# Kernel tuning notes

Measured on AMD Instinct MI355X. Metric: run time of the kernel, lower is better.

The kernel has to match this reference:

```python
import jax, jax.numpy as jnp
import numpy as np

SENTINEL = 1 << 20  # fill value for padded unique rows; far outside real coord range


def setup_inputs() -> dict:
    key = jax.random.key(0)
    k1, k2, k3, k4, k5, kw = jax.random.split(key, 6)
    M, C = 400000, 128
    voxel_features = jax.random.normal(k1, (M, C), dtype=jnp.float32)
    # coords: (batch_idx, z, y, x)
    b = jax.random.randint(k2, (M, 1), 0, 4, dtype=jnp.int32)
    z = jax.random.randint(k3, (M, 1), 0, 40, dtype=jnp.int32)
    y = jax.random.randint(k4, (M, 1), 0, 1024, dtype=jnp.int32)
    x = jax.random.randint(k5, (M, 1), 0, 1024, dtype=jnp.int32)
    voxel_coords = jnp.concatenate([b, z, y, x], axis=1)
    # layer-1 (stride=1) uses a random (in,out) matmul weight in the original;
    # materialize it as a fixed parameter for determinism.
    W0 = jax.random.normal(kw, (C, C), dtype=jnp.float32)
    return {"voxel_features": voxel_features, "voxel_coords": voxel_coords,
            "W0": W0, "batch_size": 4}


def _forward(voxel_features, W0, voxel_coords):
    M = voxel_features.shape[0]
    # layer 1: stride=1 -> relu then matmul (placeholder dense path)
    feats = jnp.maximum(voxel_features, 0.0) @ W0  # (M, 128)
    coords = voxel_coords
    # layers 2 and 3: stride=2 -> quantize coords (ALL 4 cols, incl. batch idx,
    # matching the original), unique, scatter-add features, relu
    for _ in range(2):
        coords = jnp.floor(coords.astype(jnp.float32) / 2.0).astype(jnp.int32)
        uniq, inv = jnp.unique(coords, axis=0, return_inverse=True,
                               size=M, fill_value=SENTINEL)
        inv = inv.reshape(-1)
        feats = jax.ops.segment_sum(feats, inv, num_segments=M)  # fused scatter-add
        feats = jnp.maximum(feats, 0.0)
        coords = uniq
    # rows beyond the true unique count are zero padding (sentinel coords)
    return feats


def reference(voxel_features, voxel_coords, W0, batch_size):
    return _forward(voxel_features, W0, voxel_coords)
```

## Files before the change

kernel.cpp:

```cpp
#include <hip/hip_runtime.h>
#include <stdint.h>

#define C 128

typedef __attribute__((ext_vector_type(8))) short bf16x8;
typedef __attribute__((ext_vector_type(4))) float f32x4;
typedef __attribute__((ext_vector_type(2))) float f32x2;

__device__ __forceinline__ uint32_t f2bf1(float f) {
    uint32_t u = __float_as_uint(f);
    return (u + 0x7FFFu + ((u >> 16) & 1u)) >> 16;
}


__global__ __launch_bounds__(512) void zeroconv_kernel(
    uint4* __restrict__ zbase, int nquads,
    const float* __restrict__ W, ushort* __restrict__ Wt, int nzb) {
    int b = blockIdx.x, t = threadIdx.x;
    if (b < nzb) {
        int i = b * 512 + t;
        if (i < nquads) zbase[i] = (uint4){0u, 0u, 0u, 0u};
    } else {
        int id = (b - nzb) * 512 + t;
        int n = id >> 7, k = id & 127;
        Wt[id] = (ushort)f2bf1(W[k * C + n]);
    }
}

__global__ __launch_bounds__(512) void mark_kernel(
    const int* __restrict__ coords, uint32_t* __restrict__ bm1,
    uint32_t* __restrict__ bm2, int M) {
    int i = blockIdx.x * 512 + threadIdx.x;
    if (i >= M) return;
    int bb = coords[4*i+0], z = coords[4*i+1], y = coords[4*i+2], x = coords[4*i+3];
    uint32_t k1 = ((uint32_t)(bb>>1)<<23) | ((uint32_t)(z>>1)<<18) |
                  ((uint32_t)(y>>1)<<9)  | (uint32_t)(x>>1);
    uint32_t k2 = ((uint32_t)(z>>2)<<16) | ((uint32_t)(y>>2)<<8) | (uint32_t)(x>>2);
    atomicOr(&bm1[k1>>5], 1u << (k1 & 31));
    atomicOr(&bm2[k2>>5], 1u << (k2 & 31));
}

__device__ __forceinline__ void bscan1_512(const uint32_t* bm, uint32_t* bs,
                                           int blk, uint32_t* s, int t) {
    int base = blk * 1024 + t * 2;
    uint32_t sum = __popc(bm[base]) + __popc(bm[base+1]);
    s[t] = sum;
    __syncthreads();
    for (int off = 256; off > 0; off >>= 1) {
        if (t < off) s[t] += s[t + off];
        __syncthreads();
    }
    if (t == 0) bs[blk] = s[0];
}

__device__ __forceinline__ void bscan3_512(const uint32_t* bm, const uint32_t* bs,
                                           uint32_t* wp, int blk, uint32_t* s, int t) {
    int base = blk * 1024 + t * 2;
    uint32_t p0 = __popc(bm[base]), p1 = __popc(bm[base+1]);
    uint32_t sum = p0 + p1;
    s[t] = sum;
    __syncthreads();
    for (int off = 1; off < 512; off <<= 1) {
        uint32_t add = (t >= off) ? s[t - off] : 0u;
        __syncthreads();
        s[t] += add;
        __syncthreads();
    }
    uint32_t ex = s[t] - sum + bs[blk];
    wp[base]   = ex;
    wp[base+1] = ex + p0;
}

__device__ __forceinline__ void blksum_scan_512(uint32_t* bs, uint32_t* total,
                                                int nb, uint32_t* s, int t) {
    uint32_t v = (t < nb) ? bs[t] : 0u;
    s[t] = v;
    __syncthreads();
    for (int off = 1; off < 512; off <<= 1) {
        uint32_t add = (t >= off) ? s[t - off] : 0u;
        __syncthreads();
        s[t] += add;
        __syncthreads();
    }
    if (t < nb) bs[t] = s[t] - v;
    if (t == nb - 1) *total = s[t];
}

__device__ __forceinline__ void vscan1_512(const uint32_t* v, uint32_t* bs,
                                           int blk, int n, uint32_t* s, int t) {
    int base = blk * 1024 + t * 2;
    uint32_t sum = 0;
    if (base     < n) sum += v[base];
    if (base + 1 < n) sum += v[base+1];
    s[t] = sum;
    __syncthreads();
    for (int off = 256; off > 0; off >>= 1) {
        if (t < off) s[t] += s[t + off];
        __syncthreads();
    }
    if (t == 0) bs[blk] = s[0];
}

__device__ __forceinline__ void vscan3_512(const uint32_t* v, const uint32_t* bs,
                                           uint32_t* ex_out, int blk, int n,
                                           uint32_t* s, int t) {
    int base = blk * 1024 + t * 2;
    uint32_t p0 = (base     < n) ? v[base]   : 0u;
    uint32_t p1 = (base + 1 < n) ? v[base+1] : 0u;
    uint32_t sum = p0 + p1;
    s[t] = sum;
    __syncthreads();
    for (int off = 1; off < 512; off <<= 1) {
        uint32_t add = (t >= off) ? s[t - off] : 0u;
        __syncthreads();
        s[t] += add;
        __syncthreads();
    }
    uint32_t e = s[t] - sum + bs[blk];
    if (base     < n) ex_out[base]   = e;
    if (base + 1 < n) ex_out[base+1] = e + p0;
}

__global__ __launch_bounds__(512) void mscan1_kernel(
    const uint32_t* __restrict__ bm1, uint32_t* __restrict__ bs1,
    const uint32_t* __restrict__ bm2, uint32_t* __restrict__ bs2) {
    __shared__ uint32_t s[512];
    int b = blockIdx.x, t = threadIdx.x;
    if (b < 512) bscan1_512(bm1, bs1, b, s, t);
    else         bscan1_512(bm2, bs2, b - 512, s, t);
}

__global__ __launch_bounds__(512) void mscan2_kernel(
    uint32_t* __restrict__ bs1, uint32_t* __restrict__ bs2,
    uint32_t* __restrict__ totals) {
    __shared__ uint32_t s[512];
    int t = threadIdx.x;
    if (blockIdx.x == 0) blksum_scan_512(bs1, &totals[0], 512, s, t);
    else                 blksum_scan_512(bs2, &totals[1], 32,  s, t);
}

__global__ __launch_bounds__(512) void mscan3_kernel(
    const uint32_t* __restrict__ bm1, const uint32_t* __restrict__ bs1,
    uint32_t* __restrict__ wp1,
    const uint32_t* __restrict__ bm2, const uint32_t* __restrict__ bs2,
    uint32_t* __restrict__ wp2) {
    __shared__ uint32_t s[512];
    int b = blockIdx.x, t = threadIdx.x;
    if (b < 512) bscan3_512(bm1, bs1, wp1, b, s, t);
    else         bscan3_512(bm2, bs2, wp2, b - 512, s, t);
}

__global__ __launch_bounds__(512) void count_kernel(
    const int* __restrict__ coords, const uint32_t* __restrict__ bm1,
    const uint32_t* __restrict__ wp1, uint32_t* __restrict__ counts,
    uint32_t* __restrict__ rank1_arr, uint32_t* __restrict__ slot1, int M) {
    int i = blockIdx.x * 512 + threadIdx.x;
    if (i >= M) return;
    int b = coords[4*i+0], z = coords[4*i+1], y = coords[4*i+2], x = coords[4*i+3];
    uint32_t k1 = ((uint32_t)(b>>1)<<23) | ((uint32_t)(z>>1)<<18) |
                  ((uint32_t)(y>>1)<<9)  | (uint32_t)(x>>1);
    uint32_t r1 = wp1[k1>>5] + __popc(bm1[k1>>5] & ((1u << (k1 & 31)) - 1u));
    rank1_arr[i] = r1;
    slot1[i] = atomicAdd(&counts[r1], 1u);
}

__global__ __launch_bounds__(512) void mk1_kernel(
    const uint32_t* __restrict__ counts, uint32_t* __restrict__ bsc,
    const uint32_t* __restrict__ bm1, const uint32_t* __restrict__ wp1,
    const uint32_t* __restrict__ bm2, const uint32_t* __restrict__ wp2,
    uint32_t* __restrict__ parent_r2, uint32_t* __restrict__ rowcounts2,
    uint32_t* __restrict__ childbase, int M, int nbc, int nwords) {
    int b = blockIdx.x, t = threadIdx.x;
    if (b < nbc) {
        __shared__ uint32_t s[512];
        vscan1_512(counts, bsc, b, M, s, t);
        return;
    }
    int w = (b - nbc) * 512 + t;
    if (w >= nwords) return;
    uint32_t bits = bm1[w];
    if (!bits) return;
    uint32_t r1 = wp1[w];
    while (bits) {
        int bit = __ffs(bits) - 1;
        uint32_t k1 = ((uint32_t)w << 5) | (uint32_t)bit;
        uint32_t z1 = (k1 >> 18) & 31u, y1 = (k1 >> 9) & 511u, x1 = k1 & 511u;
        uint32_t k2 = ((z1 >> 1) << 16) | ((y1 >> 1) << 8) | (x1 >> 1);
        uint32_t word2 = bm2[k2 >> 5];
        uint32_t r2 = wp2[k2 >> 5] + __popc(word2 & ((1u << (k2 & 31)) - 1u));
        parent_r2[r1] = r2;
        childbase[r1] = atomicAdd(&rowcounts2[r2], counts[r1]);
        r1++;
        bits &= bits - 1;
    }
}

__global__ __launch_bounds__(512) void mk2_kernel(
    uint32_t* __restrict__ bsc, uint32_t* __restrict__ totals,
    const uint32_t* __restrict__ rowcounts2, uint32_t* __restrict__ bsc2,
    int M, int nbc) {
    __shared__ uint32_t s[512];
    int b = blockIdx.x, t = threadIdx.x;
    if (b == 0) blksum_scan_512(bsc, &totals[2], nbc, s, t);
    else        vscan1_512(rowcounts2, bsc2, b - 1, M, s, t);
}

__global__ __launch_bounds__(512) void mk3_kernel(
    const uint32_t* __restrict__ counts, const uint32_t* __restrict__ bsc,
    uint32_t* __restrict__ start1,
    uint32_t* __restrict__ bsc2, uint32_t* __restrict__ totals,
    int M, int nbc) {
    __shared__ uint32_t s[512];
    int b = blockIdx.x, t = threadIdx.x;
    if (b < nbc) vscan3_512(counts, bsc, start1, b, M, s, t);
    else         blksum_scan_512(bsc2, &totals[3], nbc, s, t);
}

__global__ __launch_bounds__(512) void mk4_kernel(
    const uint32_t* __restrict__ rank1_arr, const uint32_t* __restrict__ start1,
    const uint32_t* __restrict__ slot1, uint32_t* __restrict__ perm,
    const uint32_t* __restrict__ rowcounts2, const uint32_t* __restrict__ bsc2,
    uint32_t* __restrict__ rowstart2, int M, int npb, int nbc) {
    int b = blockIdx.x, t = threadIdx.x;
    if (b < npb) {
        int i = b * 512 + t;
        if (i >= M) return;
        uint32_t r1 = rank1_arr[i];
        perm[start1[r1] + slot1[i]] = i;
        return;
    }
    __shared__ uint32_t s[512];
    vscan3_512(rowcounts2, bsc2, rowstart2, b - npb, M, s, t);
}

__global__ __launch_bounds__(512) void flatten_kernel(
    const uint32_t* __restrict__ parent_r2, const uint32_t* __restrict__ counts,
    const uint32_t* __restrict__ start1, const uint32_t* __restrict__ rowstart2,
    const uint32_t* __restrict__ childbase, const uint32_t* __restrict__ perm,
    uint32_t* __restrict__ perm_f, const uint32_t* __restrict__ totals, int M) {
    int i = blockIdx.x * 512 + threadIdx.x;
    if (i >= M) return;
    uint32_t U1 = totals[0];
    if ((uint32_t)i >= U1) return;
    uint32_t r2 = parent_r2[i];
    uint32_t cnt = counts[i];
    uint32_t dst = rowstart2[r2] + childbase[i];
    uint32_t s = start1[i];
    perm_f[dst] = perm[s] | 0x80000000u;
    for (uint32_t q = 1; q < cnt; ++q) perm_f[dst + q] = perm[s + q];
}

__device__ __forceinline__ void gemm_loadX(const float* __restrict__ X,
                                           int tile, int lm, int kg, f32x4* pf) {
    const char* xb = (const char*)X + ((size_t)tile*16 + lm)*512 + kg*32;
    #pragma unroll
    for (int ks = 0; ks < 4; ++ks) {
        pf[2*ks]   = __builtin_nontemporal_load((const f32x4*)(xb + ks*128));
        pf[2*ks+1] = __builtin_nontemporal_load((const f32x4*)(xb + ks*128 + 16));
    }
}

__device__ __forceinline__ void gemm_compute(const f32x4* pf, const char* wbase,
                                             ushort* __restrict__ g, int tile,
                                             int lm, int kg) {
    bf16x8 af[4];
    #pragma unroll
    for (int ks = 0; ks < 4; ++ks) {
        f32x4 a = pf[2*ks], b = pf[2*ks+1];
        union { uint32_t u[4]; bf16x8 v; } cv;
        cv.u[0] = f2bf1(fmaxf(a[0],0.f)) | (f2bf1(fmaxf(a[1],0.f)) << 16);
        cv.u[1] = f2bf1(fmaxf(a[2],0.f)) | (f2bf1(fmaxf(a[3],0.f)) << 16);
        cv.u[2] = f2bf1(fmaxf(b[0],0.f)) | (f2bf1(fmaxf(b[1],0.f)) << 16);
        cv.u[3] = f2bf1(fmaxf(b[2],0.f)) | (f2bf1(fmaxf(b[3],0.f)) << 16);
        af[ks] = cv.v;
    }
    ushort* grow = g + (size_t)((size_t)tile*16 + 4*kg)*128 + lm;
    #pragma unroll
    for (int n = 0; n < 8; ++n) {
        bf16x8 b0 = *(const bf16x8*)(wbase + n*256);
        bf16x8 b1 = *(const bf16x8*)(wbase + n*256 + 8192);
        bf16x8 b2 = *(const bf16x8*)(wbase + n*256 + 16384);
        bf16x8 b3 = *(const bf16x8*)(wbase + n*256 + 24576);
        f32x4 acc = (f32x4){0.f, 0.f, 0.f, 0.f};
        acc = __builtin_amdgcn_mfma_f32_16x16x32_bf16(af[0], b0, acc, 0, 0, 0);
        acc = __builtin_amdgcn_mfma_f32_16x16x32_bf16(af[1], b1, acc, 0, 0, 0);
        acc = __builtin_amdgcn_mfma_f32_16x16x32_bf16(af[2], b2, acc, 0, 0, 0);
        acc = __builtin_amdgcn_mfma_f32_16x16x32_bf16(af[3], b3, acc, 0, 0, 0);
        #pragma unroll
        for (int r = 0; r < 4; ++r)
            grow[(size_t)r*128 + 16*n] = (ushort)f2bf1(acc[r]);
    }
}

__global__ __launch_bounds__(256) void gemm_kernel(
    const float* __restrict__ X, const ushort* __restrict__ Wt,
    ushort* __restrict__ g, int M) {
    __shared__ __align__(16) ushort wlds[16384];
    const int t = threadIdx.x;
    {
        int sm = t & 15, kc = t >> 4;
        const char* src = (const char*)Wt;
        char* dst = (char*)wlds;
        #pragma unroll
        for (int n = 0; n < 8; ++n) {
            uint4 v = *(const uint4*)(src + n*4096 + sm*256 + kc*16);
            *(uint4*)(dst + (kc>>2)*8192 + (kc&3)*2048 + n*256 + sm*16) = v;
        }
    }
    __syncthreads();
    const int l = t & 63;
    const int lm = l & 15, kg = l >> 4;
    const int ntiles = M >> 4;
    const int nw = gridDim.x * 4;
    int tile = blockIdx.x * 4 + (t >> 6);
    const char* wbase = (const char*)wlds + kg*2048 + lm*16;

    f32x4 pfA[8], pfB[8];
    if (tile < ntiles)      gemm_loadX(X, tile, lm, kg, pfA);
    if (tile + nw < ntiles) gemm_loadX(X, tile + nw, lm, kg, pfB);
    while (true) {
        if (tile >= ntiles) break;
        gemm_compute(pfA, wbase, g, tile, lm, kg);
        if (tile + 2*nw < ntiles) gemm_loadX(X, tile + 2*nw, lm, kg, pfA);
        tile += nw;
        if (tile >= ntiles) break;
        gemm_compute(pfB, wbase, g, tile, lm, kg);
        if (tile + 2*nw < ntiles) gemm_loadX(X, tile + 2*nw, lm, kg, pfB);
        tile += nw;
    }
}

__global__ __launch_bounds__(256) void gather2_kernel(
    const uint32_t* __restrict__ rowstart2, const uint32_t* __restrict__ rowcounts2,
    const uint32_t* __restrict__ perm_f, const ushort* __restrict__ g,
    float* __restrict__ out, int M) {
    int wid = (blockIdx.x * 256 + threadIdx.x) >> 6;
    wid = __builtin_amdgcn_readfirstlane(wid);
    int lane = threadIdx.x & 63;
    if (wid >= M) return;
    const uint32_t* G = (const uint32_t*)g;
    float accx = 0.f, accy = 0.f;
    uint32_t n = rowcounts2[wid];
    if (n) {
        uint32_t s = rowstart2[wid];
        uint32_t ev = (lane < (int)n) ? perm_f[s + lane] : 0u;
        float sx = 0.f, sy = 0.f;
        uint32_t ecur = (uint32_t)__shfl((int)ev, 0);
        uint32_t pk = G[(size_t)(ecur & 0x7FFFFFFFu) * 64 + lane];
        for (uint32_t q = 1; q < n; ++q) {
            uint32_t en = (q < 64u) ? (uint32_t)__shfl((int)ev, (int)q)
                                    : perm_f[s + q];
            uint32_t pkn = G[(size_t)(en & 0x7FFFFFFFu) * 64 + lane];
            sx += __uint_as_float(pk << 16);
            sy += __uint_as_float(pk & 0xFFFF0000u);
            if (en >> 31) {
                accx += fmaxf(sx, 0.f); accy += fmaxf(sy, 0.f);
                sx = 0.f; sy = 0.f;
            }
            pk = pkn;
        }
        sx += __uint_as_float(pk << 16);
        sy += __uint_as_float(pk & 0xFFFF0000u);
        accx += fmaxf(sx, 0.f);
        accy += fmaxf(sy, 0.f);
    }
    f32x2 o; o[0] = accx; o[1] = accy;
    __builtin_nontemporal_store(o, (f32x2*)out + (size_t)wid * 64 + lane);
}

extern "C" void kernel_launch(void* const* d_in, const int* in_sizes, int n_in,
                              void* d_out, int out_size, void* d_ws, size_t ws_size,
                              hipStream_t stream) {
    const float* X      = (const float*)d_in[0];
    const int*   coords = (const int*)d_in[1];
    const float* W      = (const float*)d_in[2];
    const int M = in_sizes[0] / C;

    const int NW1 = 1 << 19;
    const int NW2 = 1 << 15;
    const int NBC = (M + 1023) / 1024;
    const int NPB = (M + 511) / 512;

    char* ws = (char*)d_ws;
    size_t off = 0;
    ushort*   g         = (ushort*)(ws + off);   off += (size_t)M * C * 2;
    uint32_t* bm1       = (uint32_t*)(ws + off); off += (size_t)NW1 * 4;
    uint32_t* bm2       = (uint32_t*)(ws + off); off += (size_t)NW2 * 4;
    uint32_t* counts    = (uint32_t*)(ws + off); off += (size_t)M * 4;
    uint32_t* rowcounts2= (uint32_t*)(ws + off); off += (size_t)M * 4;
    const size_t zero_off   = (size_t)M * C * 2;
    const size_t zero_bytes = off - zero_off;
    uint32_t* wp1       = (uint32_t*)(ws + off); off += (size_t)NW1 * 4;
    uint32_t* wp2       = (uint32_t*)(ws + off); off += (size_t)NW2 * 4;
    uint32_t* bs1       = (uint32_t*)(ws + off); off += 512 * 4;
    uint32_t* bs2       = (uint32_t*)(ws + off); off += 512 * 4;
    uint32_t* bsc       = (uint32_t*)(ws + off); off += 512 * 4;
    uint32_t* bsc2      = (uint32_t*)(ws + off); off += 512 * 4;
    uint32_t* totals    = (uint32_t*)(ws + off); off += 4 * 4;
    uint32_t* start1    = (uint32_t*)(ws + off); off += (size_t)M * 4;
    uint32_t* rank1_arr = (uint32_t*)(ws + off); off += (size_t)M * 4;
    uint32_t* slot1     = (uint32_t*)(ws + off); off += (size_t)M * 4;
    uint32_t* perm      = (uint32_t*)(ws + off); off += (size_t)M * 4;
    uint32_t* parent_r2 = (uint32_t*)(ws + off); off += (size_t)M * 4;
    uint32_t* childbase = (uint32_t*)(ws + off); off += (size_t)M * 4;
    uint32_t* rowstart2 = (uint32_t*)(ws + off); off += (size_t)M * 4;
    ushort*   Wt        = (ushort*)(ws + off);   off += (size_t)C * C * 2;
    uint32_t* perm_f    = rank1_arr;

    const int NQ  = (int)(zero_bytes / 16);
    const int NZB = (NQ + 511) / 512;

    zeroconv_kernel<<<NZB + 32, 512, 0, stream>>>((uint4*)(ws + zero_off), NQ, W, Wt, NZB);
    mark_kernel<<<NPB, 512, 0, stream>>>(coords, bm1, bm2, M);
    mscan1_kernel<<<544, 512, 0, stream>>>(bm1, bs1, bm2, bs2);
    mscan2_kernel<<<2, 512, 0, stream>>>(bs1, bs2, totals);
    mscan3_kernel<<<544, 512, 0, stream>>>(bm1, bs1, wp1, bm2, bs2, wp2);
    count_kernel<<<NPB, 512, 0, stream>>>(coords, bm1, wp1, counts, rank1_arr, slot1, M);
    mk1_kernel<<<NBC + NW1/512, 512, 0, stream>>>(counts, bsc, bm1, wp1, bm2, wp2,
                                                  parent_r2, rowcounts2, childbase,
                                                  M, NBC, NW1);
    mk2_kernel<<<1 + NBC, 512, 0, stream>>>(bsc, totals, rowcounts2, bsc2, M, NBC);
    mk3_kernel<<<NBC + 1, 512, 0, stream>>>(counts, bsc, start1, bsc2, totals, M, NBC);
    mk4_kernel<<<NPB + NBC, 512, 0, stream>>>(rank1_arr, start1, slot1, perm,
                                              rowcounts2, bsc2, rowstart2, M, NPB, NBC);
    flatten_kernel<<<NPB, 512, 0, stream>>>(
        parent_r2, counts, start1, rowstart2, childbase, perm, perm_f, totals, M);
    gemm_kernel<<<1280, 256, 0, stream>>>(X, Wt, g, M);
    gather2_kernel<<<(M + 3) / 4, 256, 0, stream>>>(
        rowstart2, rowcounts2, perm_f, g, (float*)d_out, M);
}
```

Baseline: 245.6 us.

## Replace three-pass scans with single-pass decoupled lookback and fuse flatten into GEMM

The three-phase block scans (reduce, scan of block sums, downsweep) for both bitmaps and for the count arrays become single-pass scans. Blocks take a ticket and use decoupled lookback over 64-bit flag/value state words. The flatten step is folded into the GEMM launch as extra blocks, and coordinate loads become int4 vector loads. This cuts the number of kernel launches and dependent passes over small arrays. In exchange it adds spin-waiting on global atomics and relies on ticket order for forward progress.

After: 562.1 us. 129% more time.

```diff
diff --git a/kernel.cpp b/kernel.cpp
--- a/kernel.cpp
+++ b/kernel.cpp
@@ -6,12 +6,111 @@
 typedef __attribute__((ext_vector_type(8))) short bf16x8;
 typedef __attribute__((ext_vector_type(4))) float f32x4;
 typedef __attribute__((ext_vector_type(2))) float f32x2;
+typedef unsigned long long u64;
+
+#define LBMASK 0x3FFFFFFFFFFFFFFFull
 
 __device__ __forceinline__ uint32_t f2bf1(float f) {
     uint32_t u = __float_as_uint(f);
     return (u + 0x7FFFu + ((u >> 16) & 1u)) >> 16;
 }
 
+
+__device__ __forceinline__ uint32_t lookback_wait(u64* state, int p) {
+    uint64_t run = 0; int i = p - 1;
+    while (true) {
+        u64 v = __hip_atomic_load(&state[i], __ATOMIC_ACQUIRE, __HIP_MEMORY_SCOPE_AGENT);
+        uint32_t f = (uint32_t)(v >> 62);
+        if (f == 2u) { run += (uint32_t)(v & LBMASK); break; }
+        if (f == 1u) { run += (uint32_t)(v & LBMASK); --i; }
+    }
+    return (uint32_t)run;
+}
+
+__device__ void scan_bm_lookback(const uint32_t* __restrict__ bm,
+                                 uint32_t* __restrict__ wp,
+                                 u64* state, uint32_t* ticket, int np,
+                                 uint32_t* total) {
+    __shared__ uint32_t s[512];
+    __shared__ uint32_t p_s, run_s;
+    int t = threadIdx.x;
+    if (t == 0) p_s = atomicAdd(ticket, 1u);
+    __syncthreads();
+    int p = (int)p_s;
+    int base = p * 1024 + t * 2;
+    uint32_t p0 = __popc(bm[base]), p1 = __popc(bm[base+1]);
+    uint32_t sum = p0 + p1;
+    s[t] = sum;
+    __syncthreads();
+    for (int off = 1; off < 512; off <<= 1) {
+        uint32_t add = (t >= off) ? s[t - off] : 0u;
+        __syncthreads();
+        s[t] += add;
+        __syncthreads();
+    }
+    uint32_t incl = s[t], S = s[511];
+    if (t == 0) {
+        if (p == 0) {
+            __hip_atomic_store(&state[0], (2ull << 62) | (u64)S,
+                               __ATOMIC_RELEASE, __HIP_MEMORY_SCOPE_AGENT);
+            run_s = 0;
+        } else {
+            __hip_atomic_store(&state[p], (1ull << 62) | (u64)S,
+                               __ATOMIC_RELEASE, __HIP_MEMORY_SCOPE_AGENT);
+            uint32_t run = lookback_wait(state, p);
+            __hip_atomic_store(&state[p], (2ull << 62) | (u64)(run + S),
+                               __ATOMIC_RELEASE, __HIP_MEMORY_SCOPE_AGENT);
+            run_s = run;
+        }
+    }
+    __syncthreads();
+    uint32_t ex = run_s + incl - sum;
+    wp[base]   = ex;
+    wp[base+1] = ex + p0;
+    if (total && p == np - 1 && t == 511) *total = run_s + S;
+}
+
+__device__ void scan_vals_lookback(const uint32_t* __restrict__ v,
+                                   uint32_t* __restrict__ ex_out,
+                                   u64* state, uint32_t* ticket, int np, int n) {
+    __shared__ uint32_t s[512];
+    __shared__ uint32_t p_s, run_s;
+    int t = threadIdx.x;
+    if (t == 0) p_s = atomicAdd(ticket, 1u);
+    __syncthreads();
+    int p = (int)p_s;
+    int base = p * 1024 + t * 2;
+    uint32_t p0 = (base     < n) ? v[base]   : 0u;
+    uint32_t p1 = (base + 1 < n) ? v[base+1] : 0u;
+    uint32_t sum = p0 + p1;
+    s[t] = sum;
+    __syncthreads();
+    for (int off = 1; off < 512; off <<= 1) {
+        uint32_t add = (t >= off) ? s[t - off] : 0u;
+        __syncthreads();
+        s[t] += add;
+        __syncthreads();
+    }
+    uint32_t incl = s[t], S = s[511];
+    if (t == 0) {
+        if (p == 0) {
+            __hip_atomic_store(&state[0], (2ull << 62) | (u64)S,
+                               __ATOMIC_RELEASE, __HIP_MEMORY_SCOPE_AGENT);
+            run_s = 0;
+        } else {
+            __hip_atomic_store(&state[p], (1ull << 62) | (u64)S,
+                               __ATOMIC_RELEASE, __HIP_MEMORY_SCOPE_AGENT);
+            uint32_t run = lookback_wait(state, p);
+            __hip_atomic_store(&state[p], (2ull << 62) | (u64)(run + S),
+                               __ATOMIC_RELEASE, __HIP_MEMORY_SCOPE_AGENT);
+            run_s = run;
+        }
+    }
+    __syncthreads();
+    uint32_t e = run_s + incl - sum;
+    if (base     < n) ex_out[base]   = e;
+    if (base + 1 < n) ex_out[base+1] = e + p0;
+}
 
 __global__ __launch_bounds__(512) void zeroconv_kernel(
     uint4* __restrict__ zbase, int nquads,
@@ -32,122 +131,21 @@
     uint32_t* __restrict__ bm2, int M) {
     int i = blockIdx.x * 512 + threadIdx.x;
     if (i >= M) return;
-    int bb = coords[4*i+0], z = coords[4*i+1], y = coords[4*i+2], x = coords[4*i+3];
-    uint32_t k1 = ((uint32_t)(bb>>1)<<23) | ((uint32_t)(z>>1)<<18) |
-                  ((uint32_t)(y>>1)<<9)  | (uint32_t)(x>>1);
-    uint32_t k2 = ((uint32_t)(z>>2)<<16) | ((uint32_t)(y>>2)<<8) | (uint32_t)(x>>2);
+    int4 c = ((const int4*)coords)[i];
+    uint32_t k1 = ((uint32_t)(c.x>>1)<<23) | ((uint32_t)(c.y>>1)<<18) |
+                  ((uint32_t)(c.z>>1)<<9)  | (uint32_t)(c.w>>1);
+    uint32_t k2 = ((uint32_t)(c.y>>2)<<16) | ((uint32_t)(c.z>>2)<<8) | (uint32_t)(c.w>>2);
     atomicOr(&bm1[k1>>5], 1u << (k1 & 31));
     atomicOr(&bm2[k2>>5], 1u << (k2 & 31));
 }
 
-__device__ __forceinline__ void bscan1_512(const uint32_t* bm, uint32_t* bs,
-                                           int blk, uint32_t* s, int t) {
-    int base = blk * 1024 + t * 2;
-    uint32_t sum = __popc(bm[base]) + __popc(bm[base+1]);
-    s[t] = sum;
-    __syncthreads();
-    for (int off = 256; off > 0; off >>= 1) {
-        if (t < off) s[t] += s[t + off];
-        __syncthreads();
-    }
-    if (t == 0) bs[blk] = s[0];
-}
-
-__device__ __forceinline__ void bscan3_512(const uint32_t* bm, const uint32_t* bs,
-                                           uint32_t* wp, int blk, uint32_t* s, int t) {
-    int base = blk * 1024 + t * 2;
-    uint32_t p0 = __popc(bm[base]), p1 = __popc(bm[base+1]);
-    uint32_t sum = p0 + p1;
-    s[t] = sum;
-    __syncthreads();
-    for (int off = 1; off < 512; off <<= 1) {
-        uint32_t add = (t >= off) ? s[t - off] : 0u;
-        __syncthreads();
-        s[t] += add;
-        __syncthreads();
-    }
-    uint32_t ex = s[t] - sum + bs[blk];
-    wp[base]   = ex;
-    wp[base+1] = ex + p0;
-}
-
-__device__ __forceinline__ void blksum_scan_512(uint32_t* bs, uint32_t* total,
-                                                int nb, uint32_t* s, int t) {
-    uint32_t v = (t < nb) ? bs[t] : 0u;
-    s[t] = v;
-    __syncthreads();
-    for (int off = 1; off < 512; off <<= 1) {
-        uint32_t add = (t >= off) ? s[t - off] : 0u;
-        __syncthreads();
-        s[t] += add;
-        __syncthreads();
-    }
-    if (t < nb) bs[t] = s[t] - v;
-    if (t == nb - 1) *total = s[t];
-}
-
-__device__ __forceinline__ void vscan1_512(const uint32_t* v, uint32_t* bs,
-                                           int blk, int n, uint32_t* s, int t) {
-    int base = blk * 1024 + t * 2;
-    uint32_t sum = 0;
-    if (base     < n) sum += v[base];
-    if (base + 1 < n) sum += v[base+1];
-    s[t] = sum;
-    __syncthreads();
-    for (int off = 256; off > 0; off >>= 1) {
-        if (t < off) s[t] += s[t + off];
-        __syncthreads();
-    }
-    if (t == 0) bs[blk] = s[0];
-}
-
-__device__ __forceinline__ void vscan3_512(const uint32_t* v, const uint32_t* bs,
-                                           uint32_t* ex_out, int blk, int n,
-                                           uint32_t* s, int t) {
-    int base = blk * 1024 + t * 2;
-    uint32_t p0 = (base     < n) ? v[base]   : 0u;
-    uint32_t p1 = (base + 1 < n) ? v[base+1] : 0u;
-    uint32_t sum = p0 + p1;
-    s[t] = sum;
-    __syncthreads();
-    for (int off = 1; off < 512; off <<= 1) {
-        uint32_t add = (t >= off) ? s[t - off] : 0u;
-        __syncthreads();
-        s[t] += add;
-        __syncthreads();
-    }
-    uint32_t e = s[t] - sum + bs[blk];
-    if (base     < n) ex_out[base]   = e;
-    if (base + 1 < n) ex_out[base+1] = e + p0;
-}
-
-__global__ __launch_bounds__(512) void mscan1_kernel(
-    const uint32_t* __restrict__ bm1, uint32_t* __restrict__ bs1,
-    const uint32_t* __restrict__ bm2, uint32_t* __restrict__ bs2) {
-    __shared__ uint32_t s[512];
-    int b = blockIdx.x, t = threadIdx.x;
-    if (b < 512) bscan1_512(bm1, bs1, b, s, t);
-    else         bscan1_512(bm2, bs2, b - 512, s, t);
-}
-
-__global__ __launch_bounds__(512) void mscan2_kernel(
-    uint32_t* __restrict__ bs1, uint32_t* __restrict__ bs2,
-    uint32_t* __restrict__ totals) {
-    __shared__ uint32_t s[512];
-    int t = threadIdx.x;
-    if (blockIdx.x == 0) blksum_scan_512(bs1, &totals[0], 512, s, t);
-    else                 blksum_scan_512(bs2, &totals[1], 32,  s, t);
-}
-
-__global__ __launch_bounds__(512) void mscan3_kernel(
-    const uint32_t* __restrict__ bm1, const uint32_t* __restrict__ bs1,
-    uint32_t* __restrict__ wp1,
-    const uint32_t* __restrict__ bm2, const uint32_t* __restrict__ bs2,
-    uint32_t* __restrict__ wp2) {
-    __shared__ uint32_t s[512];
-    int b = blockIdx.x, t = threadIdx.x;
-    if (b < 512) bscan3_512(bm1, bs1, wp1, b, s, t);
-    else         bscan3_512(bm2, bs2, wp2, b - 512, s, t);
+__global__ __launch_bounds__(512) void scanbm_kernel(
+    const uint32_t* __restrict__ bm1, uint32_t* __restrict__ wp1,
+    u64* st1, uint32_t* tk1,
+    const uint32_t* __restrict__ bm2, uint32_t* __restrict__ wp2,
+    u64* st2, uint32_t* tk2, uint32_t* totals) {
+    if (blockIdx.x < 512) scan_bm_lookback(bm1, wp1, st1, tk1, 512, &totals[0]);
+    else                  scan_bm_lookback(bm2, wp2, st2, tk2, 32, nullptr);
 }
 
 __global__ __launch_bounds__(512) void count_kernel(
@@ -156,27 +154,27 @@
     uint32_t* __restrict__ rank1_arr, uint32_t* __restrict__ slot1, int M) {
     int i = blockIdx.x * 512 + threadIdx.x;
     if (i >= M) return;
-    int b = coords[4*i+0], z = coords[4*i+1], y = coords[4*i+2], x = coords[4*i+3];
-    uint32_t k1 = ((uint32_t)(b>>1)<<23) | ((uint32_t)(z>>1)<<18) |
-                  ((uint32_t)(y>>1)<<9)  | (uint32_t)(x>>1);
+    int4 c = ((const int4*)coords)[i];
+    uint32_t k1 = ((uint32_t)(c.x>>1)<<23) | ((uint32_t)(c.y>>1)<<18) |
+                  ((uint32_t)(c.z>>1)<<9)  | (uint32_t)(c.w>>1);
     uint32_t r1 = wp1[k1>>5] + __popc(bm1[k1>>5] & ((1u << (k1 & 31)) - 1u));
     rank1_arr[i] = r1;
     slot1[i] = atomicAdd(&counts[r1], 1u);
 }
 
-__global__ __launch_bounds__(512) void mk1_kernel(
-    const uint32_t* __restrict__ counts, uint32_t* __restrict__ bsc,
+__global__ __launch_bounds__(512) void k5_kernel(
+    const uint32_t* __restrict__ counts, uint32_t* __restrict__ start1,
+    u64* stC, uint32_t* tkC, int M, int nbc,
     const uint32_t* __restrict__ bm1, const uint32_t* __restrict__ wp1,
     const uint32_t* __restrict__ bm2, const uint32_t* __restrict__ wp2,
     uint32_t* __restrict__ parent_r2, uint32_t* __restrict__ rowcounts2,
-    uint32_t* __restrict__ childbase, int M, int nbc, int nwords) {
-    int b = blockIdx.x, t = threadIdx.x;
+    uint32_t* __restrict__ childbase, int nwords) {
+    int b = blockIdx.x;
     if (b < nbc) {
-        __shared__ uint32_t s[512];
-        vscan1_512(counts, bsc, b, M, s, t);
+        scan_vals_lookback(counts, start1, stC, tkC, nbc, M);
         return;
     }
-    int w = (b - nbc) * 512 + t;
+    int w = (b - nbc) * 512 + threadIdx.x;
     if (w >= nwords) return;
     uint32_t bits = bm1[w];
     if (!bits) return;
@@ -195,59 +193,20 @@
     }
 }
 
-__global__ __launch_bounds__(512) void mk2_kernel(
-    uint32_t* __restrict__ bsc, uint32_t* __restrict__ totals,
-    const uint32_t* __restrict__ rowcounts2, uint32_t* __restrict__ bsc2,
-    int M, int nbc) {
-    __shared__ uint32_t s[512];
-    int b = blockIdx.x, t = threadIdx.x;
-    if (b == 0) blksum_scan_512(bsc, &totals[2], nbc, s, t);
-    else        vscan1_512(rowcounts2, bsc2, b - 1, M, s, t);
-}
-
-__global__ __launch_bounds__(512) void mk3_kernel(
-    const uint32_t* __restrict__ counts, const uint32_t* __restrict__ bsc,
-    uint32_t* __restrict__ start1,
-    uint32_t* __restrict__ bsc2, uint32_t* __restrict__ totals,
-    int M, int nbc) {
-    __shared__ uint32_t s[512];
-    int b = blockIdx.x, t = threadIdx.x;
-    if (b < nbc) vscan3_512(counts, bsc, start1, b, M, s, t);
-    else         blksum_scan_512(bsc2, &totals[3], nbc, s, t);
-}
-
-__global__ __launch_bounds__(512) void mk4_kernel(
+__global__ __launch_bounds__(512) void k6_kernel(
+    const uint32_t* __restrict__ rowcounts2, uint32_t* __restrict__ rowstart2,
+    u64* stR, uint32_t* tkR, int nbc, int M,
     const uint32_t* __restrict__ rank1_arr, const uint32_t* __restrict__ start1,
-    const uint32_t* __restrict__ slot1, uint32_t* __restrict__ perm,
-    const uint32_t* __restrict__ rowcounts2, const uint32_t* __restrict__ bsc2,
-    uint32_t* __restrict__ rowstart2, int M, int npb, int nbc) {
-    int b = blockIdx.x, t = threadIdx.x;
-    if (b < npb) {
-        int i = b * 512 + t;
-        if (i >= M) return;
-        uint32_t r1 = rank1_arr[i];
-        perm[start1[r1] + slot1[i]] = i;
+    const uint32_t* __restrict__ slot1, uint32_t* __restrict__ perm) {
+    int b = blockIdx.x;
+    if (b < nbc) {
+        scan_vals_lookback(rowcounts2, rowstart2, stR, tkR, nbc, M);
         return;
     }
-    __shared__ uint32_t s[512];
-    vscan3_512(rowcounts2, bsc2, rowstart2, b - npb, M, s, t);
-}
-
-__global__ __launch_bounds__(512) void flatten_kernel(
-    const uint32_t* __restrict__ parent_r2, const uint32_t* __restrict__ counts,
-    const uint32_t* __restrict__ start1, const uint32_t* __restrict__ rowstart2,
-    const uint32_t* __restrict__ childbase, const uint32_t* __restrict__ perm,
-    uint32_t* __restrict__ perm_f, const uint32_t* __restrict__ totals, int M) {
-    int i = blockIdx.x * 512 + threadIdx.x;
+    int i = (b - nbc) * 512 + threadIdx.x;
     if (i >= M) return;
-    uint32_t U1 = totals[0];
-    if ((uint32_t)i >= U1) return;
-    uint32_t r2 = parent_r2[i];
-    uint32_t cnt = counts[i];
-    uint32_t dst = rowstart2[r2] + childbase[i];
-    uint32_t s = start1[i];
-    perm_f[dst] = perm[s] | 0x80000000u;
-    for (uint32_t q = 1; q < cnt; ++q) perm_f[dst + q] = perm[s + q];
+    uint32_t r1 = rank1_arr[i];
+    perm[start1[r1] + slot1[i]] = i;
 }
 
 __device__ __forceinline__ void gemm_loadX(const float* __restrict__ X,
@@ -292,11 +251,30 @@
     }
 }
 
-__global__ __launch_bounds__(256) void gemm_kernel(
+__global__ __launch_bounds__(256) void gemmflat_kernel(
     const float* __restrict__ X, const ushort* __restrict__ Wt,
-    ushort* __restrict__ g, int M) {
+    ushort* __restrict__ g, int M, int nflat, int ngemm,
+    const uint32_t* __restrict__ parent_r2, const uint32_t* __restrict__ counts,
+    const uint32_t* __restrict__ start1, const uint32_t* __restrict__ rowstart2,
+    const uint32_t* __restrict__ childbase, const uint32_t* __restrict__ perm,
+    uint32_t* __restrict__ perm_f, const uint32_t* __restrict__ totals) {
+    int b = blockIdx.x;
+    const int t = threadIdx.x;
+    if (b < nflat) {
+        int i = b * 256 + t;
+        if (i >= M) return;
+        uint32_t U1 = totals[0];
+        if ((uint32_t)i >= U1) return;
+        uint32_t r2 = parent_r2[i];
+        uint32_t cnt = counts[i];
+        uint32_t dst = rowstart2[r2] + childbase[i];
+        uint32_t s = start1[i];
+        perm_f[dst] = perm[s] | 0x80000000u;
+        for (uint32_t q = 1; q < cnt; ++q) perm_f[dst + q] = perm[s + q];
+        return;
+    }
     __shared__ __align__(16) ushort wlds[16384];
-    const int t = threadIdx.x;
+    const int gb = b - nflat;
     {
         int sm = t & 15, kc = t >> 4;
         const char* src = (const char*)Wt;
@@ -311,8 +289,8 @@
     const int l = t & 63;
     const int lm = l & 15, kg = l >> 4;
     const int ntiles = M >> 4;
-    const int nw = gridDim.x * 4;
-    int tile = blockIdx.x * 4 + (t >> 6);
+    const int nw = ngemm * 4;
+    int tile = gb * 4 + (t >> 6);
     const char* wbase = (const char*)wlds + kg*2048 + lm*16;
 
     f32x4 pfA[8], pfB[8];
@@ -380,6 +358,8 @@
     const int NW2 = 1 << 15;
     const int NBC = (M + 1023) / 1024;
     const int NPB = (M + 511) / 512;
+    const int NF  = (M + 255) / 256;
+    const int NGEMM = 1280;
 
     char* ws = (char*)d_ws;
     size_t off = 0;
@@ -388,14 +368,15 @@
     uint32_t* bm2       = (uint32_t*)(ws + off); off += (size_t)NW2 * 4;
     uint32_t* counts    = (uint32_t*)(ws + off); off += (size_t)M * 4;
     uint32_t* rowcounts2= (uint32_t*)(ws + off); off += (size_t)M * 4;
+    uint32_t* ticks     = (uint32_t*)(ws + off); off += 16;
+    u64*      st1       = (u64*)(ws + off);      off += 512 * 8;
+    u64*      st2       = (u64*)(ws + off);      off += 32 * 8;
+    u64*      stC       = (u64*)(ws + off);      off += 392 * 8;
+    u64*      stR       = (u64*)(ws + off);      off += 392 * 8;
     const size_t zero_off   = (size_t)M * C * 2;
     const size_t zero_bytes = off - zero_off;
     uint32_t* wp1       = (uint32_t*)(ws + off); off += (size_t)NW1 * 4;
     uint32_t* wp2       = (uint32_t*)(ws + off); off += (size_t)NW2 * 4;
-    uint32_t* bs1       = (uint32_t*)(ws + off); off += 512 * 4;
-    uint32_t* bs2       = (uint32_t*)(ws + off); off += 512 * 4;
-    uint32_t* bsc       = (uint32_t*)(ws + off); off += 512 * 4;
-    uint32_t* bsc2      = (uint32_t*)(ws + off); off += 512 * 4;
     uint32_t* totals    = (uint32_t*)(ws + off); off += 4 * 4;
     uint32_t* start1    = (uint32_t*)(ws + off); off += (size_t)M * 4;
     uint32_t* rank1_arr = (uint32_t*)(ws + off); off += (size_t)M * 4;
@@ -412,20 +393,17 @@
 
     zeroconv_kernel<<<NZB + 32, 512, 0, stream>>>((uint4*)(ws + zero_off), NQ, W, Wt, NZB);
     mark_kernel<<<NPB, 512, 0, stream>>>(coords, bm1, bm2, M);
-    mscan1_kernel<<<544, 512, 0, stream>>>(bm1, bs1, bm2, bs2);
-    mscan2_kernel<<<2, 512, 0, stream>>>(bs1, bs2, totals);
-    mscan3_kernel<<<544, 512, 0, stream>>>(bm1, bs1, wp1, bm2, bs2, wp2);
+    scanbm_kernel<<<544, 512, 0, stream>>>(bm1, wp1, st1, &ticks[0],
+                                           bm2, wp2, st2, &ticks[1], totals);
     count_kernel<<<NPB, 512, 0, stream>>>(coords, bm1, wp1, counts, rank1_arr, slot1, M);
-    mk1_kernel<<<NBC + NW1/512, 512, 0, stream>>>(counts, bsc, bm1, wp1, bm2, wp2,
-                                                  parent_r2, rowcounts2, childbase,
-                                                  M, NBC, NW1);
-    mk2_kernel<<<1 + NBC, 512, 0, stream>>>(bsc, totals, rowcounts2, bsc2, M, NBC);
-    mk3_kernel<<<NBC + 1, 512, 0, stream>>>(counts, bsc, start1, bsc2, totals, M, NBC);
-    mk4_kernel<<<NPB + NBC, 512, 0, stream>>>(rank1_arr, start1, slot1, perm,
-                                              rowcounts2, bsc2, rowstart2, M, NPB, NBC);
-    flatten_kernel<<<NPB, 512, 0, stream>>>(
-        parent_r2, counts, start1, rowstart2, childbase, perm, perm_f, totals, M);
-    gemm_kernel<<<1280, 256, 0, stream>>>(X, Wt, g, M);
+    k5_kernel<<<NBC + NW1/512, 512, 0, stream>>>(counts, start1, stC, &ticks[2], M, NBC,
+                                                 bm1, wp1, bm2, wp2,
+                                                 parent_r2, rowcounts2, childbase, NW1);
+    k6_kernel<<<NBC + NPB, 512, 0, stream>>>(rowcounts2, rowstart2, stR, &ticks[3],
+                                             NBC, M, rank1_arr, start1, slot1, perm);
+    gemmflat_kernel<<<NF + NGEMM, 256, 0, stream>>>(X, Wt, g, M, NF, NGEMM,
+                                                    parent_r2, counts, start1, rowstart2,
+                                                    childbase, perm, perm_f, totals);
     gather2_kernel<<<(M + 3) / 4, 256, 0, stream>>>(
         rowstart2, rowcounts2, perm_f, g, (float*)d_out, M);
 }
```
